# Kernel tuning notes

Measured on AMD Instinct MI355X. Metric: run time of the kernel, lower is better.

Reference implementation:

```python
import jax, jax.numpy as jnp
import numpy as np

H, W = 256, 336
FLOW_SCALING = float(max(H, W))  # max(config['loader']['resolution'])
REG_WEIGHT = 0.001               # config['loss']['flow_regul_weight']
B, N = 8, 262144


def setup_inputs() -> dict:
    key = jax.random.key(0)
    k1, k2, k3, k4, k5 = jax.random.split(key, 5)
    # small flow so a reasonable fraction of warped events stays in-bounds
    flow = 0.05 * jax.random.normal(k1, (B, 2, H, W), dtype=jnp.float32)
    ys = jax.random.randint(k2, (B, N), 0, H).astype(jnp.float32)
    xs = jax.random.randint(k3, (B, N), 0, W).astype(jnp.float32)
    ts = jax.random.uniform(k4, (B, N), dtype=jnp.float32)  # normalized timestamps in [0,1]
    pol = jax.random.randint(k5, (B, N), 0, 2)
    # event layout per the code: (ts, y, x, p)
    event_list = jnp.stack([ts, ys, xs, pol.astype(jnp.float32) * 2.0 - 1.0], axis=-1)
    pol_mask = jnp.stack([(pol == 1), (pol == 0)], axis=-1).astype(jnp.float32)  # [B,N,2]
    return {"flow": flow, "event_list": event_list, "pol_mask": pol_mask}


def _get_interpolation(events, event_flow, tref):
    # warped event coords (y, x): [B, N, 2]
    warped = events[:, :, 1:3] + (tref - events[:, :, 0:1]) * event_flow * FLOW_SCALING
    top_y = jnp.floor(warped[:, :, 0:1])
    bot_y = jnp.floor(warped[:, :, 0:1] + 1.0)
    left_x = jnp.floor(warped[:, :, 1:2])
    right_x = jnp.floor(warped[:, :, 1:2] + 1.0)
    # four bilinear corners stacked along event dim -> [B, 4N, 2]
    idx = jnp.concatenate([
        jnp.concatenate([top_y, left_x], -1),
        jnp.concatenate([top_y, right_x], -1),
        jnp.concatenate([bot_y, left_x], -1),
        jnp.concatenate([bot_y, right_x], -1)], axis=1)
    warped4 = jnp.tile(warped, (1, 4, 1))
    weights = jnp.maximum(0.0, 1.0 - jnp.abs(warped4 - idx))
    mask = ((idx[:, :, 0:1] >= 0) & (idx[:, :, 0:1] < H)
            & (idx[:, :, 1:2] >= 0) & (idx[:, :, 1:2] < W)).astype(weights.dtype)
    idx = idx * mask          # unfeasible indices -> 0
    weights = weights * mask  # unfeasible weights -> 0
    flat_idx = (idx[:, :, 0] * W + idx[:, :, 1]).astype(jnp.int32)  # [B, 4N]
    w = jnp.prod(weights, axis=-1, keepdims=True)                    # [B, 4N, 1]
    return flat_idx, w


def _interpolate(flat_idx, weights, polarity_mask):
    # scatter-add bilinear weights into an H*W image, per batch element
    w = (weights * polarity_mask)[:, :, 0]  # [B, 4N]
    return jax.vmap(lambda i, v: jax.ops.segment_sum(v, i, num_segments=H * W))(flat_idx, w)


def reference(flow, event_list, pol_mask):
    pol4 = jnp.tile(pol_mask, (1, 4, 1))              # [B, 4N, 2]
    ts4 = jnp.tile(event_list[:, :, 0:1], (1, 4, 1))  # [B, 4N, 1]
    # gather flow at original event pixel locations
    flow_idx = (event_list[:, :, 1] * W + event_list[:, :, 2]).astype(jnp.int32)  # [B, N]
    flow_flat = flow.reshape(flow.shape[0], 2, -1)
    event_flowy = jnp.take_along_axis(flow_flat[:, 1, :], flow_idx, axis=1)
    event_flowx = jnp.take_along_axis(flow_flat[:, 0, :], flow_idx, axis=1)
    event_flow = jnp.stack([event_flowy, event_flowx], axis=-1)  # [B, N, 2] (y, x)

    loss = jnp.float32(0.0)
    # forward warp (tref=1, avg ts) and backward warp (tref=0, avg 1-ts)
    for tref, tgrad in ((1.0, ts4), (0.0, 1.0 - ts4)):
        idx, wts = _get_interpolation(event_list, event_flow, tref)
        for p in range(2):  # positive / negative polarity
            pm = pol4[:, :, p:p + 1]
            iwe = _interpolate(idx, wts, pm)
            iwe_ts = _interpolate(idx, wts * tgrad, pm)
            loss = loss + jnp.sum((iwe_ts / (iwe + 1e-9)) ** 2)

    # charbonnier flow smoothness
    flow_dx = flow[:, :, :-1, :] - flow[:, :, 1:, :]
    flow_dy = flow[:, :, :, :-1] - flow[:, :, :, 1:]
    smooth = jnp.sum(jnp.sqrt(flow_dx ** 2 + 1e-6)) + jnp.sum(jnp.sqrt(flow_dy ** 2 + 1e-6))
    return loss + REG_WEIGHT * smooth
```

## Files before the change

kernel.cpp:

```cpp
#include <hip/hip_runtime.h>

#define HH 256
#define WW 336
#define HWPIX (HH * WW)
#define BATCH 8
#define NEV 262144
#define NEV_SHIFT 18
#define FLOW_SCALING 336.0f
#define REG_WEIGHT 0.001f

#define BANDS 16
#define BANDSHIFT 4
#define BANDROWS 16
#define NBINS (2 * BATCH * BANDS)
#define CAP 20480
#define GSTRIDE 16

#define BE_THREADS 512
#define EVPT 2
#define EV_PER_BLOCK (BE_THREADS * EVPT)
#define MAXITEMS 4096

#define HALFROWS 8
#define HTILE (HALFROWS * WW)
#define NBLK_ACC (BANDS * 2 * 2 * BATCH)

#define GCOUNT_BYTES (NBINS * GSTRIDE * 4)
#define ITEMS_BYTES ((size_t)NBINS * CAP * 8)

__device__ __forceinline__ float wave_reduce_sum(float v) {
    #pragma unroll
    for (int o = 32; o > 0; o >>= 1) v += __shfl_down(v, o, 64);
    return v;
}

__device__ __forceinline__ float charb(float d) { return sqrtf(d * d + 1e-6f); }

__global__ __launch_bounds__(256)
void flow_prep(const float* __restrict__ flow, float2* __restrict__ flowi,
               unsigned int* __restrict__ gcount, float* __restrict__ loss_acc,
               unsigned int* __restrict__ done_count,
               float* __restrict__ smooth_partial) {
    __shared__ float red[4];
    int tid = threadIdx.x;
    if (blockIdx.x == 0) {
        for (int i = tid; i < NBINS * GSTRIDE; i += 256) gcount[i] = 0u;
        if (tid == 0) { *loss_acc = 0.0f; *done_count = 0u; }
    }

    const int N4 = BATCH * HWPIX / 4;
    const int H4 = HWPIX / 4;
    const int W4 = WW / 4;
    float v = 0.0f;
    for (int i = blockIdx.x * 256 + tid; i < N4; i += gridDim.x * 256) {
        int b = i / H4, u = i - b * H4;
        int row = u / W4, c4 = u - row * W4;
        const float4* ch0 = (const float4*)(flow + (size_t)b * 2 * HWPIX);
        const float4* ch1 = ch0 + H4;
        float4 a0 = ch0[u];
        float4 a1 = ch1[u];

        float4* fo = (float4*)(flowi + (size_t)b * HWPIX);
        fo[2 * u]     = make_float4(a0.x, a1.x, a0.y, a1.y);
        fo[2 * u + 1] = make_float4(a0.z, a1.z, a0.w, a1.w);

        if (row < HH - 1) {
            float4 d0 = ch0[u + W4];
            float4 d1 = ch1[u + W4];
            v += charb(a0.x - d0.x) + charb(a0.y - d0.y) +
                 charb(a0.z - d0.z) + charb(a0.w - d0.w) +
                 charb(a1.x - d1.x) + charb(a1.y - d1.y) +
                 charb(a1.z - d1.z) + charb(a1.w - d1.w);
        }
        v += charb(a0.x - a0.y) + charb(a0.y - a0.z) + charb(a0.z - a0.w) +
             charb(a1.x - a1.y) + charb(a1.y - a1.z) + charb(a1.z - a1.w);
        if (c4 < W4 - 1) {
            float r0 = ((const float*)ch0)[4 * u + 4];
            float r1 = ((const float*)ch1)[4 * u + 4];
            v += charb(a0.w - r0) + charb(a1.w - r1);
        }
    }
    v = wave_reduce_sum(v);
    if ((tid & 63) == 0) red[tid >> 6] = v;
    __syncthreads();
    if (tid < 4) {
        float r = red[tid];
        r += __shfl_down(r, 2, 64);
        r += __shfl_down(r, 1, 64);
        if (tid == 0) smooth_partial[blockIdx.x] = r;
    }
}

__global__ __launch_bounds__(BE_THREADS)
void bin_events(const float2* __restrict__ flowi,
                const float4* __restrict__ ev,
                unsigned int* __restrict__ gcount,
                uint2* __restrict__ items) {
    __shared__ int lcnt[32];
    __shared__ int loff[32];
    __shared__ int gbase[32];
    __shared__ int stotal;
    __shared__ __align__(16) unsigned long long sval[MAXITEMS];

    int tid = threadIdx.x;
    if (tid < 32) lcnt[tid] = 0;
    __syncthreads();

    int base = blockIdx.x * EV_PER_BLOCK;
    int b = base >> NEV_SHIFT;
    const float2* fB = flowi + (size_t)b * HWPIX;

    unsigned int pkv[EVPT][2];
    unsigned int hiA[EVPT][2], hiB[EVPT][2];
    int rkA[EVPT][2], rkB[EVPT][2];

    #pragma unroll
    for (int e = 0; e < EVPT; ++e) {
        int bn = base + e * BE_THREADS + tid;
        float4 ee = ev[bn];
        float t = ee.x, y = ee.y, x = ee.z;
        unsigned int p = (ee.w > 0.0f) ? 0u : 1u;

        int iy = (int)y, ix = (int)x;
        float2 f = fB[iy * WW + ix];
        float fx = f.x, fy = f.y;

        #pragma unroll
        for (int tr = 0; tr < 2; ++tr) {
            rkA[e][tr] = -1; rkB[e][tr] = -1;
            float tref  = tr ? 0.0f : 1.0f;
            float tg    = tr ? (1.0f - t) : t;
            float dtS = (tref - t) * FLOW_SCALING;
            float wy = fmaf(dtS, fy, y);
            float wx = fmaf(dtS, fx, x);
            if (!(wx > -1.0f && wx < (float)WW)) continue;
            if (!(wy > -1.0f && wy < (float)HH)) continue;

            int ty = (int)floorf(wy);
            int band0 = -1, band1 = -1;
            if (ty >= 0 && ty < HH) band0 = ty >> BANDSHIFT;
            int r1 = ty + 1;
            if (r1 >= 0 && r1 < HH) {
                int bb = r1 >> BANDSHIFT;
                if (bb != band0) band1 = bb;
            }

            unsigned int qx = (unsigned int)(fmaf(wx, 2048.0f, 2048.5f));
            unsigned int qt = (unsigned int)(tg * 2047.0f + 0.5f);
            pkv[e][tr] = (qx << 12) | (qt << 1) | p;

            if (band0 >= 0) {
                float wyrel = wy - (float)(band0 * BANDROWS - 1);
                unsigned int qy = (unsigned int)fmaf(wyrel, 2048.0f, 0.5f);
                int lb = tr * BANDS + band0;
                hiA[e][tr] = qy | ((unsigned int)lb << 16);
                rkA[e][tr] = atomicAdd(&lcnt[lb], 1);
            }
            if (band1 >= 0) {
                float wyrel = wy - (float)(band1 * BANDROWS - 1);
                unsigned int qy = (unsigned int)fmaf(wyrel, 2048.0f, 0.5f);
                int lb = tr * BANDS + band1;
                hiB[e][tr] = qy | ((unsigned int)lb << 16);
                rkB[e][tr] = atomicAdd(&lcnt[lb], 1);
            }
        }
    }
    __syncthreads();

    if (tid < 32) {
        int c = lcnt[tid];
        int xg = c;
        #pragma unroll
        for (int o = 1; o < 32; o <<= 1) {
            int yv = __shfl_up(xg, o, 64);
            if (tid >= o) xg += yv;
        }
        loff[tid] = xg - c;
        if (tid == 31) stotal = xg;
        int gbin = (tid >> 4) * (BATCH * BANDS) + b * BANDS + (tid & 15);
        gbase[tid] = c > 0 ? (int)atomicAdd(&gcount[gbin * GSTRIDE],
                                            (unsigned int)c) : 0;
    }
    __syncthreads();

    #pragma unroll
    for (int e = 0; e < EVPT; ++e) {
        #pragma unroll
        for (int tr = 0; tr < 2; ++tr) {
            if (rkA[e][tr] >= 0) {
                int lb = (hiA[e][tr] >> 16) & 31;
                sval[loff[lb] + rkA[e][tr]] =
                    (unsigned long long)pkv[e][tr] |
                    ((unsigned long long)hiA[e][tr] << 32);
            }
            if (rkB[e][tr] >= 0) {
                int lb = (hiB[e][tr] >> 16) & 31;
                sval[loff[lb] + rkB[e][tr]] =
                    (unsigned long long)pkv[e][tr] |
                    ((unsigned long long)hiB[e][tr] << 32);
            }
        }
    }
    __syncthreads();

    int total = stotal;
    for (int i = tid * 2; i < total; i += 2 * BE_THREADS) {
        uint4 two = *(const uint4*)&sval[i];
        unsigned int pk0 = two.x, h0 = two.y;
        unsigned int qy0 = h0 & 0xffffu;
        int lb0 = (h0 >> 16) & 31;
        int gs0 = gbase[lb0] + (i - loff[lb0]);
        int gbin0 = (lb0 >> 4) * (BATCH * BANDS) + b * BANDS + (lb0 & 15);

        if ((i + 1) < total) {
            unsigned int pk1 = two.z, h1 = two.w;
            unsigned int qy1 = h1 & 0xffffu;
            int lb1 = (h1 >> 16) & 31;
            int gs1 = gbase[lb1] + (i + 1 - loff[lb1]);
            if (lb1 == lb0 && (gs0 & 1) == 0 && gs1 < CAP) {
                *(uint4*)(items + (size_t)gbin0 * CAP + gs0) =
                    make_uint4(pk0, qy0, pk1, qy1);
                continue;
            }
            int gbin1 = (lb1 >> 4) * (BATCH * BANDS) + b * BANDS + (lb1 & 15);
            if (gs1 < CAP) items[(size_t)gbin1 * CAP + gs1] = make_uint2(pk1, qy1);
        }
        if (gs0 < CAP) items[(size_t)gbin0 * CAP + gs0] = make_uint2(pk0, qy0);
    }
}

__device__ __forceinline__ unsigned int pack_w(float w, float tg) {
    unsigned int lo16 = (unsigned int)fmaf(w, 1024.0f, 0.5f);
    unsigned int hi16 = (unsigned int)fmaf(w * tg, 1024.0f, 0.5f);
    return lo16 | (hi16 << 16);
}

__device__ __forceinline__ void accum_item(unsigned int* __restrict__ sA,
                                           unsigned int* __restrict__ sB,
                                           unsigned int pk, unsigned int qy,
                                           int half) {
    float wx = (float)(pk >> 12) * (1.0f / 2048.0f) - 1.0f;
    float tg = (float)((pk >> 1) & 2047u) * (1.0f / 2047.0f);
    int p = pk & 1u;

    int rowq = qy >> 11;
    float fy = (float)(qy & 2047u) * (1.0f / 2048.0f);
    int row_top = rowq - 1;

    float lxf = floorf(wx);
    float fxx = wx - lxf;
    int lx = (int)lxf;

    unsigned int* A  = sA + p * HTILE;
    unsigned int* Bb = sB + p * HTILE;
    int rbase = half * HALFROWS;

    #pragma unroll
    for (int a = 0; a < 2; ++a) {
        int ry = row_top + a - rbase;
        if ((unsigned)ry >= (unsigned)HALFROWS) continue;
        float wrow = a ? fy : (1.0f - fy);
        int rb = ry * WW;
        if (lx >= 0 && lx + 1 < WW) {
            unsigned int pl = pack_w(wrow * (1.0f - fxx), tg);
            unsigned int pr = pack_w(wrow * fxx, tg);
            unsigned long long v =
                (unsigned long long)pl | ((unsigned long long)pr << 32);
            if ((lx & 1) == 0) {
                atomicAdd((unsigned long long*)(A + rb + lx), v);
            } else {
                atomicAdd((unsigned long long*)(Bb + rb + lx - 1), v);
            }
        } else if (lx == -1) {
            atomicAdd(&A[rb], pack_w(wrow * fxx, tg));
        } else if (lx == WW - 1) {
            atomicAdd(&A[rb + lx], pack_w(wrow * (1.0f - fxx), tg));
        }
    }
}

__global__ __launch_bounds__(1024)
void bin_accum(const unsigned int* __restrict__ gcount,
               const uint2* __restrict__ items,
               const float* __restrict__ smooth_partial,
               float* __restrict__ loss_acc,
               unsigned int* __restrict__ done_count,
               float* __restrict__ out) {
    __shared__ __align__(16) unsigned int sA[2 * HTILE];
    __shared__ __align__(16) unsigned int sB[2 * HTILE];
    __shared__ float red[16];
    __shared__ int lastflag;

    int bx   = blockIdx.x;
    int band = bx >> 1;
    int half = bx & 1;
    int tr   = blockIdx.y;
    int b    = blockIdx.z;
    int tid  = threadIdx.x;

    for (int i = tid; i < 2 * HTILE; i += 1024) { sA[i] = 0u; sB[i] = 0u; }
    __syncthreads();

    int gbin = (tr * BATCH + b) * BANDS + band;
    int cnt = min((int)gcount[gbin * GSTRIDE], CAP);
    const uint2* bp = items + (size_t)gbin * CAP;
    const uint4* bp4 = (const uint4*)bp;

    int nquad = cnt >> 2;
    for (int n = tid; n < nquad; n += 1024) {
        uint4 c0 = bp4[2 * n];
        uint4 c1 = bp4[2 * n + 1];
        accum_item(sA, sB, c0.x, c0.y, half);
        accum_item(sA, sB, c0.z, c0.w, half);
        accum_item(sA, sB, c1.x, c1.y, half);
        accum_item(sA, sB, c1.z, c1.w, half);
    }
    int rem = cnt & 3;
    if (tid < rem) {
        uint2 u = bp[nquad * 4 + tid];
        accum_item(sA, sB, u.x, u.y, half);
    }
    __syncthreads();

    float v = 0.0f;
    for (int i = tid; i < 2 * HTILE; i += 1024) {
        int px = i - (i / WW) * WW;
        unsigned int u = sA[i] + (px ? sB[i - 1] : 0u);
        float iwe = (float)(u & 0xffffu);
        float its = (float)(u >> 16);
        float r = its / (iwe + 1.024e-6f);
        v += r * r;
    }
    v = wave_reduce_sum(v);
    if ((tid & 63) == 0) red[tid >> 6] = v;
    __syncthreads();
    if (tid == 0) {
        float r = 0.0f;
        #pragma unroll
        for (int k = 0; k < 16; ++k) r += red[k];
        atomicAdd(loss_acc, r);
        __threadfence();
        unsigned int t = atomicAdd(done_count, 1u);
        lastflag = (t == (unsigned)(NBLK_ACC - 1));
    }
    __syncthreads();

    if (lastflag) {
        float pv = (tid < 512) ? smooth_partial[tid] : 0.0f;
        pv = wave_reduce_sum(pv);
        if ((tid & 63) == 0) red[tid >> 6] = pv;
        __syncthreads();
        if (tid == 0) {
            float sm = 0.0f;
            #pragma unroll
            for (int k = 0; k < 16; ++k) sm += red[k];
            float total = atomicAdd(loss_acc, 0.0f);
            *out = total + REG_WEIGHT * sm;
        }
    }
}

extern "C" void kernel_launch(void* const* d_in, const int* in_sizes, int n_in,
                              void* d_out, int out_size, void* d_ws, size_t ws_size,
                              hipStream_t stream) {
    const float*  flow  = (const float*)d_in[0];
    const float4* ev    = (const float4*)d_in[1];
    float* out = (float*)d_out;

    unsigned int* gcount     = (unsigned int*)d_ws;
    float*        loss_acc   = (float*)((char*)d_ws + GCOUNT_BYTES);
    unsigned int* done_count = (unsigned int*)((char*)d_ws + GCOUNT_BYTES + 4);
    float*        smooth_p   = (float*)((char*)d_ws + GCOUNT_BYTES + 512);
    uint2*        items      = (uint2*)((char*)d_ws + GCOUNT_BYTES + 4096);
    float2*       flowi      = (float2*)((char*)d_ws + GCOUNT_BYTES + 4096 + ITEMS_BYTES);

    flow_prep<<<512, 256, 0, stream>>>(flow, flowi, gcount, loss_acc,
                                       done_count, smooth_p);

    int total_ev = BATCH * NEV;
    bin_events<<<total_ev / EV_PER_BLOCK, BE_THREADS, 0, stream>>>(
        flowi, ev, gcount, items);

    dim3 g2(BANDS * 2, 2, BATCH);
    bin_accum<<<g2, 1024, 0, stream>>>(gcount, items, smooth_p, loss_acc,
                                       done_count, out);
}
```

Before: 148.5 us.

## Use 8-row bands so each accumulate block reads only its own bin items

```diff
diff --git a/kernel.cpp b/kernel.cpp
--- a/kernel.cpp
+++ b/kernel.cpp
@@ -9,11 +9,11 @@
 #define FLOW_SCALING 336.0f
 #define REG_WEIGHT 0.001f
 
-#define BANDS 16
-#define BANDSHIFT 4
-#define BANDROWS 16
+#define BANDS 32
+#define BANDSHIFT 3
+#define BANDROWS 8
 #define NBINS (2 * BATCH * BANDS)
-#define CAP 20480
+#define CAP 14336
 #define GSTRIDE 16
 
 #define BE_THREADS 512
@@ -21,9 +21,8 @@
 #define EV_PER_BLOCK (BE_THREADS * EVPT)
 #define MAXITEMS 4096
 
-#define HALFROWS 8
-#define HTILE (HALFROWS * WW)
-#define NBLK_ACC (BANDS * 2 * 2 * BATCH)
+#define HTILE (BANDROWS * WW)
+#define NBLK_ACC NBINS
 
 #define GCOUNT_BYTES (NBINS * GSTRIDE * 4)
 #define ITEMS_BYTES ((size_t)NBINS * CAP * 8)
@@ -37,7 +36,7 @@
 __device__ __forceinline__ float charb(float d) { return sqrtf(d * d + 1e-6f); }
 
 __global__ __launch_bounds__(256)
-void flow_prep(const float* __restrict__ flow, float2* __restrict__ flowi,
+void flow_prep(const float* __restrict__ flow,
                unsigned int* __restrict__ gcount, float* __restrict__ loss_acc,
                unsigned int* __restrict__ done_count,
                float* __restrict__ smooth_partial) {
@@ -60,10 +59,6 @@
         float4 a0 = ch0[u];
         float4 a1 = ch1[u];
 
-        float4* fo = (float4*)(flowi + (size_t)b * HWPIX);
-        fo[2 * u]     = make_float4(a0.x, a1.x, a0.y, a1.y);
-        fo[2 * u + 1] = make_float4(a0.z, a1.z, a0.w, a1.w);
-
         if (row < HH - 1) {
             float4 d0 = ch0[u + W4];
             float4 d1 = ch1[u + W4];
@@ -92,23 +87,24 @@
 }
 
 __global__ __launch_bounds__(BE_THREADS)
-void bin_events(const float2* __restrict__ flowi,
+void bin_events(const float* __restrict__ flow,
                 const float4* __restrict__ ev,
                 unsigned int* __restrict__ gcount,
                 uint2* __restrict__ items) {
-    __shared__ int lcnt[32];
-    __shared__ int loff[32];
-    __shared__ int gbase[32];
+    __shared__ int lcnt[64];
+    __shared__ int loff[64];
+    __shared__ int gbase[64];
     __shared__ int stotal;
     __shared__ __align__(16) unsigned long long sval[MAXITEMS];
 
     int tid = threadIdx.x;
-    if (tid < 32) lcnt[tid] = 0;
+    if (tid < 64) lcnt[tid] = 0;
     __syncthreads();
 
     int base = blockIdx.x * EV_PER_BLOCK;
     int b = base >> NEV_SHIFT;
-    const float2* fB = flowi + (size_t)b * HWPIX;
+    const float* fxp = flow + (size_t)b * 2 * HWPIX;
+    const float* fyp = fxp + HWPIX;
 
     unsigned int pkv[EVPT][2];
     unsigned int hiA[EVPT][2], hiB[EVPT][2];
@@ -122,8 +118,9 @@
         unsigned int p = (ee.w > 0.0f) ? 0u : 1u;
 
         int iy = (int)y, ix = (int)x;
-        float2 f = fB[iy * WW + ix];
-        float fx = f.x, fy = f.y;
+        int off = iy * WW + ix;
+        float fx = fxp[off];
+        float fy = fyp[off];
 
         #pragma unroll
         for (int tr = 0; tr < 2; ++tr) {
@@ -167,17 +164,17 @@
     }
     __syncthreads();
 
-    if (tid < 32) {
+    if (tid < 64) {
         int c = lcnt[tid];
         int xg = c;
         #pragma unroll
-        for (int o = 1; o < 32; o <<= 1) {
+        for (int o = 1; o < 64; o <<= 1) {
             int yv = __shfl_up(xg, o, 64);
             if (tid >= o) xg += yv;
         }
         loff[tid] = xg - c;
-        if (tid == 31) stotal = xg;
-        int gbin = (tid >> 4) * (BATCH * BANDS) + b * BANDS + (tid & 15);
+        if (tid == 63) stotal = xg;
+        int gbin = ((tid >> 5) * BATCH + b) * BANDS + (tid & 31);
         gbase[tid] = c > 0 ? (int)atomicAdd(&gcount[gbin * GSTRIDE],
                                             (unsigned int)c) : 0;
     }
@@ -188,13 +185,13 @@
         #pragma unroll
         for (int tr = 0; tr < 2; ++tr) {
             if (rkA[e][tr] >= 0) {
-                int lb = (hiA[e][tr] >> 16) & 31;
+                int lb = (hiA[e][tr] >> 16) & 63;
                 sval[loff[lb] + rkA[e][tr]] =
                     (unsigned long long)pkv[e][tr] |
                     ((unsigned long long)hiA[e][tr] << 32);
             }
             if (rkB[e][tr] >= 0) {
-                int lb = (hiB[e][tr] >> 16) & 31;
+                int lb = (hiB[e][tr] >> 16) & 63;
                 sval[loff[lb] + rkB[e][tr]] =
                     (unsigned long long)pkv[e][tr] |
                     ((unsigned long long)hiB[e][tr] << 32);
@@ -208,21 +205,21 @@
         uint4 two = *(const uint4*)&sval[i];
         unsigned int pk0 = two.x, h0 = two.y;
         unsigned int qy0 = h0 & 0xffffu;
-        int lb0 = (h0 >> 16) & 31;
+        int lb0 = (h0 >> 16) & 63;
         int gs0 = gbase[lb0] + (i - loff[lb0]);
-        int gbin0 = (lb0 >> 4) * (BATCH * BANDS) + b * BANDS + (lb0 & 15);
+        int gbin0 = ((lb0 >> 5) * BATCH + b) * BANDS + (lb0 & 31);
 
         if ((i + 1) < total) {
             unsigned int pk1 = two.z, h1 = two.w;
             unsigned int qy1 = h1 & 0xffffu;
-            int lb1 = (h1 >> 16) & 31;
+            int lb1 = (h1 >> 16) & 63;
             int gs1 = gbase[lb1] + (i + 1 - loff[lb1]);
             if (lb1 == lb0 && (gs0 & 1) == 0 && gs1 < CAP) {
                 *(uint4*)(items + (size_t)gbin0 * CAP + gs0) =
                     make_uint4(pk0, qy0, pk1, qy1);
                 continue;
             }
-            int gbin1 = (lb1 >> 4) * (BATCH * BANDS) + b * BANDS + (lb1 & 15);
+            int gbin1 = ((lb1 >> 5) * BATCH + b) * BANDS + (lb1 & 31);
             if (gs1 < CAP) items[(size_t)gbin1 * CAP + gs1] = make_uint2(pk1, qy1);
         }
         if (gs0 < CAP) items[(size_t)gbin0 * CAP + gs0] = make_uint2(pk0, qy0);
@@ -237,8 +234,7 @@
 
 __device__ __forceinline__ void accum_item(unsigned int* __restrict__ sA,
                                            unsigned int* __restrict__ sB,
-                                           unsigned int pk, unsigned int qy,
-                                           int half) {
+                                           unsigned int pk, unsigned int qy) {
     float wx = (float)(pk >> 12) * (1.0f / 2048.0f) - 1.0f;
     float tg = (float)((pk >> 1) & 2047u) * (1.0f / 2047.0f);
     int p = pk & 1u;
@@ -253,12 +249,11 @@
 
     unsigned int* A  = sA + p * HTILE;
     unsigned int* Bb = sB + p * HTILE;
-    int rbase = half * HALFROWS;
 
     #pragma unroll
     for (int a = 0; a < 2; ++a) {
-        int ry = row_top + a - rbase;
-        if ((unsigned)ry >= (unsigned)HALFROWS) continue;
+        int ry = row_top + a;
+        if ((unsigned)ry >= (unsigned)BANDROWS) continue;
         float wrow = a ? fy : (1.0f - fy);
         int rb = ry * WW;
         if (lx >= 0 && lx + 1 < WW) {
@@ -291,9 +286,7 @@
     __shared__ float red[16];
     __shared__ int lastflag;
 
-    int bx   = blockIdx.x;
-    int band = bx >> 1;
-    int half = bx & 1;
+    int band = blockIdx.x;
     int tr   = blockIdx.y;
     int b    = blockIdx.z;
     int tid  = threadIdx.x;
@@ -310,15 +303,15 @@
     for (int n = tid; n < nquad; n += 1024) {
         uint4 c0 = bp4[2 * n];
         uint4 c1 = bp4[2 * n + 1];
-        accum_item(sA, sB, c0.x, c0.y, half);
-        accum_item(sA, sB, c0.z, c0.w, half);
-        accum_item(sA, sB, c1.x, c1.y, half);
-        accum_item(sA, sB, c1.z, c1.w, half);
+        accum_item(sA, sB, c0.x, c0.y);
+        accum_item(sA, sB, c0.z, c0.w);
+        accum_item(sA, sB, c1.x, c1.y);
+        accum_item(sA, sB, c1.z, c1.w);
     }
     int rem = cnt & 3;
     if (tid < rem) {
         uint2 u = bp[nquad * 4 + tid];
-        accum_item(sA, sB, u.x, u.y, half);
+        accum_item(sA, sB, u.x, u.y);
     }
     __syncthreads();
 
@@ -372,16 +365,15 @@
     unsigned int* done_count = (unsigned int*)((char*)d_ws + GCOUNT_BYTES + 4);
     float*        smooth_p   = (float*)((char*)d_ws + GCOUNT_BYTES + 512);
     uint2*        items      = (uint2*)((char*)d_ws + GCOUNT_BYTES + 4096);
-    float2*       flowi      = (float2*)((char*)d_ws + GCOUNT_BYTES + 4096 + ITEMS_BYTES);
-
-    flow_prep<<<512, 256, 0, stream>>>(flow, flowi, gcount, loss_acc,
+
+    flow_prep<<<512, 256, 0, stream>>>(flow, gcount, loss_acc,
                                        done_count, smooth_p);
 
     int total_ev = BATCH * NEV;
     bin_events<<<total_ev / EV_PER_BLOCK, BE_THREADS, 0, stream>>>(
-        flowi, ev, gcount, items);
-
-    dim3 g2(BANDS * 2, 2, BATCH);
+        flow, ev, gcount, items);
+
+    dim3 g2(BANDS, 2, BATCH);
     bin_accum<<<g2, 1024, 0, stream>>>(gcount, items, smooth_p, loss_acc,
                                        done_count, out);
 }
```

Result: no change. 149.1 us (+0.4%).
